# Performance work log

Measured on AMD Instinct MI355X. Metric: run time of the kernel, lower is better.

The kernel has to match this reference:

```python
import math
import jax, jax.numpy as jnp
import numpy as np


def setup_inputs() -> dict:
    key = jax.random.key(0)
    ks = jax.random.split(key, 5)
    B, N, D, O = 16, 16384, 256, 256
    x = jax.random.normal(ks[0], (B, N, D), dtype=jnp.float32)
    Wq = jax.random.normal(ks[1], (O, D), dtype=jnp.float32) * (1.0 / math.sqrt(D))
    bq = jax.random.normal(ks[2], (O,), dtype=jnp.float32) * 0.01
    Wk = jax.random.normal(ks[3], (O, D), dtype=jnp.float32) * (1.0 / math.sqrt(D))
    bk = jax.random.normal(ks[4], (O,), dtype=jnp.float32) * 0.01
    return {"x": x, "Wq": Wq, "bq": bq, "Wk": Wk, "bk": bk}


def reference(x, Wq, bq, Wk, bk):
    # x: [B, N, D]; Wq/Wk: [O, D] (torch nn.Linear layout), bq/bk: [O]
    O = Wq.shape[0]
    scale = 1.0 / math.sqrt(O)
    q = jnp.einsum('bnd,od->bno', x, Wq) + bq          # [B, N, O]
    k = jnp.einsum('bnd,od->bno', x, Wk) + bk          # [B, N, O]
    # sum_j (q_i . k_j) == q_i . (sum_j k_j): avoid the O(N^2) score matrix
    ksum = k.sum(axis=1)                               # [B, O]
    summed_scores = jnp.einsum('bno,bo->bn', q, ksum) * scale  # [B, N]
    customer_weights = jax.nn.softmax(summed_scores, axis=-1)  # [B, N]
    aggregated_feature = jnp.einsum('bn,bnd->bd', customer_weights, x)  # [B, D]
    average_customer_weights = customer_weights.mean(axis=0)            # [N]
    return aggregated_feature, average_customer_weights
```

## Files before the change

kernel.cpp:

```cpp
#include <hip/hip_runtime.h>
#include <math.h>

#define BB 16
#define NN 16384
#define DD 256
#define NS1 128
#define NS3 128

typedef float floatx4 __attribute__((ext_vector_type(4)));

__device__ __forceinline__ floatx4 ntload4(const float* p) {
  return __builtin_nontemporal_load((const floatx4*)p);
}

__global__ __launch_bounds__(256) void k1_xsum_part(const float* __restrict__ x,
                                                    float* __restrict__ part) {
  const int b = blockIdx.y, blk = blockIdx.x;
  const int wave = threadIdx.x >> 6, lane = threadIdx.x & 63;
  const int rows = NN / NS1;
  const float* xp = x + ((size_t)b * NN + (size_t)blk * rows + wave) * DD + lane * 4;
  floatx4 a0 = {0.f, 0.f, 0.f, 0.f}, a1 = a0, a2 = a0, a3 = a0;
  floatx4 a4 = a0, a5 = a0, a6 = a0, a7 = a0;
#pragma unroll
  for (int r = 0; r < rows; r += 32) {
    a0 += ntload4(xp + (size_t)(r + 0) * DD);
    a1 += ntload4(xp + (size_t)(r + 4) * DD);
    a2 += ntload4(xp + (size_t)(r + 8) * DD);
    a3 += ntload4(xp + (size_t)(r + 12) * DD);
    a4 += ntload4(xp + (size_t)(r + 16) * DD);
    a5 += ntload4(xp + (size_t)(r + 20) * DD);
    a6 += ntload4(xp + (size_t)(r + 24) * DD);
    a7 += ntload4(xp + (size_t)(r + 28) * DD);
  }
  const floatx4 acc = ((a0 + a1) + (a2 + a3)) + ((a4 + a5) + (a6 + a7));
  __shared__ float sP[4][DD];
  *(floatx4*)&sP[wave][lane * 4] = acc;
  __syncthreads();
  const int t = threadIdx.x;
  part[((size_t)b * NS1 + blk) * DD + t] = sP[0][t] + sP[1][t] + sP[2][t] + sP[3][t];
}

__global__ __launch_bounds__(1024) void k2_prep(const float* __restrict__ part,
                                                const float* __restrict__ Wq,
                                                const float* __restrict__ bq,
                                                const float* __restrict__ Wk,
                                                const float* __restrict__ bk,
                                                float* __restrict__ v,
                                                float* __restrict__ c) {
  const int b = blockIdx.x, t = threadIdx.x;
  const int d = t & 255;
  const int g = t >> 8;
  __shared__ float stage[4][DD];
  __shared__ float xs[DD];
  __shared__ float ks[DD];
  __shared__ float red[256];

  const float* pb = part + (size_t)b * NS1 * DD + d;
  float a[8];
#pragma unroll
  for (int u = 0; u < 8; ++u) a[u] = 0.f;
#pragma unroll
  for (int blk = 0; blk < 32; blk += 8) {
#pragma unroll
    for (int u = 0; u < 8; ++u) a[u] += pb[(size_t)(g * 32 + blk + u) * DD];
  }
  stage[g][d] = ((a[0] + a[1]) + (a[2] + a[3])) + ((a[4] + a[5]) + (a[6] + a[7]));
  __syncthreads();
  if (g == 0) xs[d] = (stage[0][d] + stage[1][d]) + (stage[2][d] + stage[3][d]);
  __syncthreads();

  float kp = 0.f;
  const float4* wk4 = (const float4*)(Wk + (size_t)d * DD + g * 64);
#pragma unroll 4
  for (int j4 = 0; j4 < 16; ++j4) {
    const float4 w = wk4[j4];
    const int j = g * 64 + 4 * j4;
    kp += w.x * xs[j] + w.y * xs[j + 1] + w.z * xs[j + 2] + w.w * xs[j + 3];
  }
  stage[g][d] = kp;
  __syncthreads();
  if (g == 0)
    ks[d] = (stage[0][d] + stage[1][d]) + (stage[2][d] + stage[3][d]) + (float)NN * bk[d];
  __syncthreads();

  float vp = 0.f;
#pragma unroll 4
  for (int o = 0; o < 64; ++o)
    vp += Wq[(size_t)(g * 64 + o) * DD + d] * ks[g * 64 + o];
  stage[g][d] = vp;
  __syncthreads();
  if (g == 0) {
    v[b * DD + d] = (stage[0][d] + stage[1][d]) + (stage[2][d] + stage[3][d]);
    red[d] = bq[d] * ks[d];
  }
  __syncthreads();
  for (int s = 128; s > 0; s >>= 1) {
    if (t < s) red[t] += red[t + s];
    __syncthreads();
  }
  if (t == 0) c[b] = red[0];
}

__global__ __launch_bounds__(256) void k3_main(const float* __restrict__ x,
                                               const float* __restrict__ v,
                                               const float* __restrict__ c,
                                               float* __restrict__ scores,
                                               float* __restrict__ pm,
                                               float* __restrict__ pz,
                                               float* __restrict__ pP) {
  const int b = blockIdx.y, blk = blockIdx.x;
  const int wave = threadIdx.x >> 6, lane = threadIdx.x & 63;
  const float scale = 0.0625f;

  const floatx4 vl = *(const floatx4*)(v + b * DD + lane * 4);
  const float cb = c[b];
  const int rows_per_block = NN / NS3;
  const int rows_per_wave = rows_per_block / 4;
  const int n0 = blk * rows_per_block + wave * rows_per_wave;
  const float* xb = x + (size_t)b * NN * DD;

  float m = -INFINITY, Z = 0.f;
  floatx4 P = {0.f, 0.f, 0.f, 0.f};

#define DOT_OF(XR) ({ const floatx4 _p = (XR) * vl; _p.x + _p.y + _p.z + _p.w; })

  for (int i = 0; i < rows_per_wave; i += 8) {
    const float* base = xb + (size_t)(n0 + i) * DD + lane * 4;
    const floatx4 xr0 = ntload4(base);
    const floatx4 xr1 = ntload4(base + DD);
    const floatx4 xr2 = ntload4(base + 2 * DD);
    const floatx4 xr3 = ntload4(base + 3 * DD);
    const floatx4 xr4 = ntload4(base + 4 * DD);
    const floatx4 xr5 = ntload4(base + 5 * DD);
    const floatx4 xr6 = ntload4(base + 6 * DD);
    const floatx4 xr7 = ntload4(base + 7 * DD);
    float d0 = DOT_OF(xr0), d1 = DOT_OF(xr1), d2 = DOT_OF(xr2), d3 = DOT_OF(xr3);
    float d4 = DOT_OF(xr4), d5 = DOT_OF(xr5), d6 = DOT_OF(xr6), d7 = DOT_OF(xr7);
#pragma unroll
    for (int off = 32; off >= 1; off >>= 1) {
      d0 += __shfl_xor(d0, off, 64);
      d1 += __shfl_xor(d1, off, 64);
      d2 += __shfl_xor(d2, off, 64);
      d3 += __shfl_xor(d3, off, 64);
      d4 += __shfl_xor(d4, off, 64);
      d5 += __shfl_xor(d5, off, 64);
      d6 += __shfl_xor(d6, off, 64);
      d7 += __shfl_xor(d7, off, 64);
    }
    const float s0 = (d0 + cb) * scale, s1 = (d1 + cb) * scale;
    const float s2 = (d2 + cb) * scale, s3 = (d3 + cb) * scale;
    const float s4 = (d4 + cb) * scale, s5 = (d5 + cb) * scale;
    const float s6 = (d6 + cb) * scale, s7 = (d7 + cb) * scale;
    if (lane == 0) {
      floatx4 sva = {s0, s1, s2, s3};
      floatx4 svb = {s4, s5, s6, s7};
      *(floatx4*)(scores + (size_t)b * NN + n0 + i) = sva;
      *(floatx4*)(scores + (size_t)b * NN + n0 + i + 4) = svb;
    }
#define SM_UPDATE(S, XR)                                   \
    if ((S) > m) {                                         \
      const float alpha = __expf(m - (S));                 \
      Z = Z * alpha + 1.f;                                 \
      P = P * alpha + (XR);                                \
      m = (S);                                             \
    } else {                                               \
      const float e = __expf((S) - m);                     \
      Z += e;                                              \
      P += (XR) * e;                                       \
    }
    SM_UPDATE(s0, xr0)
    SM_UPDATE(s1, xr1)
    SM_UPDATE(s2, xr2)
    SM_UPDATE(s3, xr3)
    SM_UPDATE(s4, xr4)
    SM_UPDATE(s5, xr5)
    SM_UPDATE(s6, xr6)
    SM_UPDATE(s7, xr7)
#undef SM_UPDATE
  }

  __shared__ float sm[4], sz[4];
  __shared__ float sP[4][DD];
  *(floatx4*)&sP[wave][lane * 4] = P;
  if (lane == 0) { sm[wave] = m; sz[wave] = Z; }
  __syncthreads();

  const int t = threadIdx.x;
  const float M = fmaxf(fmaxf(sm[0], sm[1]), fmaxf(sm[2], sm[3]));
  const float e0 = __expf(sm[0] - M), e1 = __expf(sm[1] - M);
  const float e2 = __expf(sm[2] - M), e3 = __expf(sm[3] - M);
  const float Pd = sP[0][t] * e0 + sP[1][t] * e1 + sP[2][t] * e2 + sP[3][t] * e3;
  const size_t idx = (size_t)b * NS3 + blk;
  pP[idx * DD + t] = Pd;
  if (t == 0) {
    pm[idx] = M;
    pz[idx] = sz[0] * e0 + sz[1] * e1 + sz[2] * e2 + sz[3] * e3;
  }
}

__global__ __launch_bounds__(256) void k45_final(const float* __restrict__ pm,
                                                 const float* __restrict__ pz,
                                                 const float* __restrict__ pP,
                                                 const float* __restrict__ scores,
                                                 float* __restrict__ out_agg,
                                                 float* __restrict__ out_w) {
  const int t = threadIdx.x;
  if (blockIdx.x < BB) {
    const int b = blockIdx.x;
    __shared__ float red[256];
    __shared__ float sw[NS3];
    const size_t base = (size_t)b * NS3;

    red[t] = (t < NS3) ? pm[base + t] : -INFINITY;
    __syncthreads();
    for (int s = 128; s > 0; s >>= 1) {
      if (t < s) red[t] = fmaxf(red[t], red[t + s]);
      __syncthreads();
    }
    const float M = red[0];
    __syncthreads();

    const float w_t = (t < NS3) ? __expf(pm[base + t] - M) : 0.f;
    if (t < NS3) sw[t] = w_t;
    red[t] = (t < NS3) ? pz[base + t] * w_t : 0.f;
    __syncthreads();
    for (int s = 128; s > 0; s >>= 1) {
      if (t < s) red[t] += red[t + s];
      __syncthreads();
    }
    const float rZ = 1.f / red[0];

    float a0 = 0.f, a1 = 0.f, a2 = 0.f, a3 = 0.f;
    const float* pb = pP + base * DD + t;
#pragma unroll 8
    for (int blk = 0; blk < NS3; blk += 4) {
      a0 += pb[(size_t)(blk + 0) * DD] * sw[blk + 0];
      a1 += pb[(size_t)(blk + 1) * DD] * sw[blk + 1];
      a2 += pb[(size_t)(blk + 2) * DD] * sw[blk + 2];
      a3 += pb[(size_t)(blk + 3) * DD] * sw[blk + 3];
    }
    out_agg[b * DD + t] = ((a0 + a1) + (a2 + a3)) * rZ;
  } else {
    const int wb = blockIdx.x - BB;
    __shared__ float sM[BB], sR[BB];
    const int b = t >> 4;
    const int i = t & 15;
    const size_t base = (size_t)b * NS3 + i * 8;

    float mloc = -INFINITY;
#pragma unroll
    for (int k = 0; k < 8; ++k) mloc = fmaxf(mloc, pm[base + k]);
#pragma unroll
    for (int off = 8; off >= 1; off >>= 1) mloc = fmaxf(mloc, __shfl_xor(mloc, off, 64));
    const float M = mloc;

    float zloc = 0.f;
#pragma unroll
    for (int k = 0; k < 8; ++k) zloc += pz[base + k] * __expf(pm[base + k] - M);
#pragma unroll
    for (int off = 8; off >= 1; off >>= 1) zloc += __shfl_xor(zloc, off, 64);

    if (i == 0) { sM[b] = M; sR[b] = 1.f / zloc; }
    __syncthreads();

    const int n = wb * 256 + t;
    float acc = 0.f;
#pragma unroll
    for (int bb = 0; bb < BB; ++bb)
      acc += __expf(scores[(size_t)bb * NN + n] - sM[bb]) * sR[bb];
    out_w[n] = acc * (1.f / BB);
  }
}

extern "C" void kernel_launch(void* const* d_in, const int* in_sizes, int n_in,
                              void* d_out, int out_size, void* d_ws, size_t ws_size,
                              hipStream_t stream) {
  const float* x  = (const float*)d_in[0];
  const float* Wq = (const float*)d_in[1];
  const float* bq = (const float*)d_in[2];
  const float* Wk = (const float*)d_in[3];
  const float* bk = (const float*)d_in[4];

  float* out  = (float*)d_out;
  float* agg  = out;
  float* avgw = out + BB * DD;

  float* ws = (float*)d_ws;
  float* part   = ws;  ws += (size_t)BB * NS1 * DD;
  float* v      = ws;  ws += BB * DD;
  float* c      = ws;  ws += BB;
  float* scores = ws;  ws += (size_t)BB * NN;
  float* pm     = ws;  ws += BB * NS3;
  float* pz     = ws;  ws += BB * NS3;
  float* pP     = ws;  ws += (size_t)BB * NS3 * DD;

  k1_xsum_part<<<dim3(NS1, BB), 256, 0, stream>>>(x, part);
  k2_prep<<<BB, 1024, 0, stream>>>(part, Wq, bq, Wk, bk, v, c);
  k3_main<<<dim3(NS3, BB), 256, 0, stream>>>(x, v, c, scores, pm, pz, pP);
  k45_final<<<BB + NN / 256, 256, 0, stream>>>(pm, pz, pP, scores, agg, avgw);
}
```

Measured before the change: 108.9 us.

## Split each wave into half-waves processing two rows with 8-wide lanes

Restructures the main kernel so each 32-lane half-wave handles a separate row, with each lane loading 8 floats. This shortens the dot-product shuffle reduction from six steps to five and gives each lane two rows in flight per iteration. The divergent branchy online-softmax update is replaced by a branchless max/exp form, which costs two exps per row instead of one. The two halves are merged with cross-half shuffles before the block reduction. Per-wave row count is hardcoded to 32, which relies on NN/NS3 being 128.

After: 111.9 us. +2.8%, slower.

```diff
diff --git a/kernel.cpp b/kernel.cpp
--- a/kernel.cpp
+++ b/kernel.cpp
@@ -109,83 +109,87 @@
                                                float* __restrict__ pz,
                                                float* __restrict__ pP) {
   const int b = blockIdx.y, blk = blockIdx.x;
-  const int wave = threadIdx.x >> 6, lane = threadIdx.x & 63;
+  const int t = threadIdx.x;
+  const int wave = t >> 6, lane = t & 63;
+  const int hl = lane & 31;
+  const int half = lane >> 5;
   const float scale = 0.0625f;
 
-  const floatx4 vl = *(const floatx4*)(v + b * DD + lane * 4);
+  const floatx4 vl0 = *(const floatx4*)(v + b * DD + hl * 8);
+  const floatx4 vl1 = *(const floatx4*)(v + b * DD + hl * 8 + 4);
   const float cb = c[b];
   const int rows_per_block = NN / NS3;
-  const int rows_per_wave = rows_per_block / 4;
-  const int n0 = blk * rows_per_block + wave * rows_per_wave;
+  const int n0 = blk * rows_per_block + wave * 32;
   const float* xb = x + (size_t)b * NN * DD;
 
   float m = -INFINITY, Z = 0.f;
-  floatx4 P = {0.f, 0.f, 0.f, 0.f};
-
-#define DOT_OF(XR) ({ const floatx4 _p = (XR) * vl; _p.x + _p.y + _p.z + _p.w; })
-
-  for (int i = 0; i < rows_per_wave; i += 8) {
-    const float* base = xb + (size_t)(n0 + i) * DD + lane * 4;
-    const floatx4 xr0 = ntload4(base);
-    const floatx4 xr1 = ntload4(base + DD);
-    const floatx4 xr2 = ntload4(base + 2 * DD);
-    const floatx4 xr3 = ntload4(base + 3 * DD);
-    const floatx4 xr4 = ntload4(base + 4 * DD);
-    const floatx4 xr5 = ntload4(base + 5 * DD);
-    const floatx4 xr6 = ntload4(base + 6 * DD);
-    const floatx4 xr7 = ntload4(base + 7 * DD);
-    float d0 = DOT_OF(xr0), d1 = DOT_OF(xr1), d2 = DOT_OF(xr2), d3 = DOT_OF(xr3);
-    float d4 = DOT_OF(xr4), d5 = DOT_OF(xr5), d6 = DOT_OF(xr6), d7 = DOT_OF(xr7);
-#pragma unroll
-    for (int off = 32; off >= 1; off >>= 1) {
+  floatx4 P0 = {0.f, 0.f, 0.f, 0.f};
+  floatx4 P1 = {0.f, 0.f, 0.f, 0.f};
+
+  for (int i = 0; i < 32; i += 8) {
+    const float* rp0 = xb + (size_t)(n0 + i + 0 + half) * DD + hl * 8;
+    const float* rp1 = xb + (size_t)(n0 + i + 2 + half) * DD + hl * 8;
+    const float* rp2 = xb + (size_t)(n0 + i + 4 + half) * DD + hl * 8;
+    const float* rp3 = xb + (size_t)(n0 + i + 6 + half) * DD + hl * 8;
+    const floatx4 xa0 = ntload4(rp0), xc0 = ntload4(rp0 + 4);
+    const floatx4 xa1 = ntload4(rp1), xc1 = ntload4(rp1 + 4);
+    const floatx4 xa2 = ntload4(rp2), xc2 = ntload4(rp2 + 4);
+    const floatx4 xa3 = ntload4(rp3), xc3 = ntload4(rp3 + 4);
+
+#define DOT8(XA, XC) ({ const floatx4 _q0 = (XA) * vl0, _q1 = (XC) * vl1; \
+                        ((_q0.x + _q0.y) + (_q0.z + _q0.w)) + \
+                        ((_q1.x + _q1.y) + (_q1.z + _q1.w)); })
+    float d0 = DOT8(xa0, xc0), d1 = DOT8(xa1, xc1);
+    float d2 = DOT8(xa2, xc2), d3 = DOT8(xa3, xc3);
+#undef DOT8
+#pragma unroll
+    for (int off = 16; off >= 1; off >>= 1) {
       d0 += __shfl_xor(d0, off, 64);
       d1 += __shfl_xor(d1, off, 64);
       d2 += __shfl_xor(d2, off, 64);
       d3 += __shfl_xor(d3, off, 64);
-      d4 += __shfl_xor(d4, off, 64);
-      d5 += __shfl_xor(d5, off, 64);
-      d6 += __shfl_xor(d6, off, 64);
-      d7 += __shfl_xor(d7, off, 64);
     }
     const float s0 = (d0 + cb) * scale, s1 = (d1 + cb) * scale;
     const float s2 = (d2 + cb) * scale, s3 = (d3 + cb) * scale;
-    const float s4 = (d4 + cb) * scale, s5 = (d5 + cb) * scale;
-    const float s6 = (d6 + cb) * scale, s7 = (d7 + cb) * scale;
-    if (lane == 0) {
-      floatx4 sva = {s0, s1, s2, s3};
-      floatx4 svb = {s4, s5, s6, s7};
-      *(floatx4*)(scores + (size_t)b * NN + n0 + i) = sva;
-      *(floatx4*)(scores + (size_t)b * NN + n0 + i + 4) = svb;
-    }
-#define SM_UPDATE(S, XR)                                   \
-    if ((S) > m) {                                         \
-      const float alpha = __expf(m - (S));                 \
-      Z = Z * alpha + 1.f;                                 \
-      P = P * alpha + (XR);                                \
-      m = (S);                                             \
-    } else {                                               \
-      const float e = __expf((S) - m);                     \
-      Z += e;                                              \
-      P += (XR) * e;                                       \
-    }
-    SM_UPDATE(s0, xr0)
-    SM_UPDATE(s1, xr1)
-    SM_UPDATE(s2, xr2)
-    SM_UPDATE(s3, xr3)
-    SM_UPDATE(s4, xr4)
-    SM_UPDATE(s5, xr5)
-    SM_UPDATE(s6, xr6)
-    SM_UPDATE(s7, xr7)
-#undef SM_UPDATE
-  }
+    if (hl == 0) {
+      float* sc = scores + (size_t)b * NN + n0 + i + half;
+      sc[0] = s0; sc[2] = s1; sc[4] = s2; sc[6] = s3;
+    }
+#define UPD(S, XA, XC) { \
+    const float mn = fmaxf(m, (S)); \
+    const float al = __expf(m - mn); \
+    const float e  = __expf((S) - mn); \
+    Z = Z * al + e; \
+    P0 = P0 * al + (XA) * e; \
+    P1 = P1 * al + (XC) * e; \
+    m = mn; }
+    UPD(s0, xa0, xc0)
+    UPD(s1, xa1, xc1)
+    UPD(s2, xa2, xc2)
+    UPD(s3, xa3, xc3)
+#undef UPD
+  }
+
+  const float mo = __shfl_xor(m, 32, 64);
+  const float Mw = fmaxf(m, mo);
+  const float eh = __expf(m - Mw);
+  float Zp = Z * eh;
+  Zp += __shfl_xor(Zp, 32, 64);
+  floatx4 Q0 = P0 * eh, Q1 = P1 * eh;
+  Q0.x += __shfl_xor(Q0.x, 32, 64); Q0.y += __shfl_xor(Q0.y, 32, 64);
+  Q0.z += __shfl_xor(Q0.z, 32, 64); Q0.w += __shfl_xor(Q0.w, 32, 64);
+  Q1.x += __shfl_xor(Q1.x, 32, 64); Q1.y += __shfl_xor(Q1.y, 32, 64);
+  Q1.z += __shfl_xor(Q1.z, 32, 64); Q1.w += __shfl_xor(Q1.w, 32, 64);
 
   __shared__ float sm[4], sz[4];
   __shared__ float sP[4][DD];
-  *(floatx4*)&sP[wave][lane * 4] = P;
-  if (lane == 0) { sm[wave] = m; sz[wave] = Z; }
-  __syncthreads();
-
-  const int t = threadIdx.x;
+  if (half == 0) {
+    *(floatx4*)&sP[wave][hl * 8] = Q0;
+    *(floatx4*)&sP[wave][hl * 8 + 4] = Q1;
+  }
+  if (lane == 0) { sm[wave] = Mw; sz[wave] = Zp; }
+  __syncthreads();
+
   const float M = fmaxf(fmaxf(sm[0], sm[1]), fmaxf(sm[2], sm[3]));
   const float e0 = __expf(sm[0] - M), e1 = __expf(sm[1] - M);
   const float e2 = __expf(sm[2] - M), e3 = __expf(sm[3] - M);
```
